# Performance work log

Measured on AMD Instinct MI355X. Metric: run time of the kernel, lower is better.

The kernel has to match this reference:

```python
import jax, jax.numpy as jnp
import numpy as np

N_NODES = 20000
N_EDGES = 240000
IN_DIM = 20
SH_DIM = 16  # (lmax+1)^2 with lmax=3
DENOM = 1.0
EPS = 1e-12


def spherical_harmonics_lmax3(v):
    """Real spherical harmonics l=0..3 on unit vectors v: [E,3] -> [E,16]."""
    x, y, z = v[:, 0], v[:, 1], v[:, 2]
    x2, y2, z2 = x * x, y * y, z * z
    sh = [
        jnp.full_like(x, 0.28209479177387814),            # l=0
        0.4886025119029199 * y,                            # l=1, m=-1
        0.4886025119029199 * z,                            # l=1, m=0
        0.4886025119029199 * x,                            # l=1, m=1
        1.0925484305920792 * x * y,                        # l=2, m=-2
        1.0925484305920792 * y * z,                        # l=2, m=-1
        0.31539156525252005 * (3.0 * z2 - 1.0),            # l=2, m=0
        1.0925484305920792 * x * z,                        # l=2, m=1
        0.5462742152960396 * (x2 - y2),                    # l=2, m=2
        0.5900435899266435 * y * (3.0 * x2 - y2),          # l=3, m=-3
        2.890611442640554 * x * y * z,                     # l=3, m=-2
        0.4570457994644658 * y * (5.0 * z2 - 1.0),         # l=3, m=-1
        0.3731763325901154 * z * (5.0 * z2 - 3.0),         # l=3, m=0
        0.4570457994644658 * x * (5.0 * z2 - 1.0),         # l=3, m=1
        1.445305721320277 * z * (x2 - y2),                 # l=3, m=2
        0.5900435899266435 * x * (x2 - 3.0 * y2),          # l=3, m=3
    ]
    return jnp.stack(sh, axis=-1)


def setup_inputs() -> dict:
    key = jax.random.key(0)
    ks = jax.random.split(key, 10)
    x = jax.random.normal(ks[0], (N_NODES, IN_DIM), dtype=jnp.float32)
    positions = jax.random.normal(ks[1], (N_NODES, 3), dtype=jnp.float32)
    edge_index = jax.random.randint(ks[2], (2, N_EDGES), 0, N_NODES, dtype=jnp.int32)
    s = 1.0 / np.sqrt(IN_DIM)
    W_pre = jax.random.uniform(ks[3], (IN_DIM, IN_DIM), jnp.float32, -s, s)
    b_pre = jax.random.uniform(ks[4], (IN_DIM,), jnp.float32, -s, s)
    W_post = jax.random.uniform(ks[5], (IN_DIM, IN_DIM), jnp.float32, -s, s)
    b_post = jax.random.uniform(ks[6], (IN_DIM,), jnp.float32, -s, s)
    W_sc = jax.random.uniform(ks[7], (IN_DIM, IN_DIM), jnp.float32, -s, s)
    b_sc = jax.random.uniform(ks[8], (IN_DIM,), jnp.float32, -s, s)
    return {"x": x, "positions": positions, "edge_index": edge_index,
            "W_pre": W_pre, "b_pre": b_pre, "W_post": W_post, "b_post": b_post,
            "W_sc": W_sc, "b_sc": b_sc}


def reference(x, positions, edge_index, W_pre, b_pre, W_post, b_post, W_sc, b_sc):
    row, col = edge_index[0], edge_index[1]
    # per-edge gather + relative positions
    rel = positions[col] - positions[row]                      # [E,3]
    norm = jnp.sqrt(jnp.sum(rel * rel, axis=-1, keepdims=True) + EPS)
    sh = spherical_harmonics_lmax3(rel / norm)                 # [E,16]
    sender = x[row]                                            # [E,20]
    # equivariant tensor product (outer product over irreps channels)
    tp = (sender[:, :, None] * sh[:, None, :]).reshape(sender.shape[0], IN_DIM * SH_DIM)  # [E,320]
    edge_features = jnp.concatenate([sender, tp], axis=1)      # [E,340]
    # scatter-add aggregation to target nodes
    aggr = jax.ops.segment_sum(edge_features, col, num_segments=N_NODES)  # [N,340]
    # node update MLP + shortcut (math of Layer.update)
    h = x / DENOM
    h = jax.nn.relu(h @ W_pre.T + b_pre)
    h = h @ W_post.T + b_post
    out = x @ W_sc.T + b_sc + h                                # [N,20]
    # aggr is computed (and aggregated) by the original propagate; concat so it stays live
    return jnp.concatenate([out, aggr], axis=1)                # [N,360]
```

## Files before the change

kernel.cpp:

```cpp
#include <hip/hip_runtime.h>

#define N_NODES 20000
#define N_EDGES 240000
#define IN_DIM  20
#define AGG_DIM 340
#define OUT_DIM 360
#define EPS_F   1e-12f
#define CAP     64
#define EDGE_BLOCKS ((N_EDGES + 255) / 256)
#define MLP_BLOCKS  ((N_NODES + 255) / 256)

typedef _Float16 half8 __attribute__((ext_vector_type(8)));

__device__ __forceinline__ float sh_coeff(int k, float xn, float yn, float zn) {
    const float x2 = xn * xn, y2 = yn * yn, z2 = zn * zn;
    switch (k) {
        case 0:  return 0.28209479177387814f;
        case 1:  return 0.4886025119029199f * yn;
        case 2:  return 0.4886025119029199f * zn;
        case 3:  return 0.4886025119029199f * xn;
        case 4:  return 1.0925484305920792f * xn * yn;
        case 5:  return 1.0925484305920792f * yn * zn;
        case 6:  return 0.31539156525252005f * (3.0f * z2 - 1.0f);
        case 7:  return 1.0925484305920792f * xn * zn;
        case 8:  return 0.5462742152960396f * (x2 - y2);
        case 9:  return 0.5900435899266435f * yn * (3.0f * x2 - y2);
        case 10: return 2.890611442640554f  * xn * yn * zn;
        case 11: return 0.4570457994644658f * yn * (5.0f * z2 - 1.0f);
        case 12: return 0.3731763325901154f * zn * (5.0f * z2 - 3.0f);
        case 13: return 0.4570457994644658f * xn * (5.0f * z2 - 1.0f);
        case 14: return 1.445305721320277f  * zn * (x2 - y2);
        default: return 0.5900435899266435f * xn * (x2 - 3.0f * y2);
    }
}

__global__ __launch_bounds__(256) void bucket_sh_mlp(
    const float* __restrict__ pos,
    const int* __restrict__ ei,
    const float* __restrict__ x,
    const float* __restrict__ Wpre,  const float* __restrict__ bpre,
    const float* __restrict__ Wpost, const float* __restrict__ bpost,
    const float* __restrict__ Wsc,   const float* __restrict__ bsc,
    int* __restrict__ counts,
    int* __restrict__ ovf_cnt,
    int* __restrict__ ovf,
    int* __restrict__ bucket,
    half8* __restrict__ shbuf,
    float* __restrict__ out)
{
    if ((int)blockIdx.x < EDGE_BLOCKS) {
        const int e = (int)(blockIdx.x * 256 + threadIdx.x);
        if (e >= N_EDGES) return;
        const int row = ei[e];
        const int col = ei[N_EDGES + e];
        const int slot = atomicAdd(&counts[col], 1);
        if (slot >= CAP) { ovf[atomicAdd(ovf_cnt, 1)] = e; return; }

        const int sidx = col * CAP + slot;
        bucket[sidx] = row;

        const float rx = pos[col * 3 + 0] - pos[row * 3 + 0];
        const float ry = pos[col * 3 + 1] - pos[row * 3 + 1];
        const float rz = pos[col * 3 + 2] - pos[row * 3 + 2];
        const float rinv = rsqrtf(rx * rx + ry * ry + rz * rz + EPS_F);
        const float xx = rx * rinv, yy = ry * rinv, zz = rz * rinv;
        const float x2 = xx * xx, y2 = yy * yy, z2 = zz * zz;

        const float sh0  = 0.28209479177387814f;
        const float sh1  = 0.4886025119029199f * yy;
        const float sh2  = 0.4886025119029199f * zz;
        const float sh3  = 0.4886025119029199f * xx;
        const float sh4  = 1.0925484305920792f * xx * yy;
        const float sh5  = 1.0925484305920792f * yy * zz;
        const float sh6  = 0.31539156525252005f * (3.0f * z2 - 1.0f);
        const float sh7  = 1.0925484305920792f * xx * zz;
        const float sh8  = 0.5462742152960396f * (x2 - y2);
        const float sh9  = 0.5900435899266435f * yy * (3.0f * x2 - y2);
        const float sh10 = 2.890611442640554f  * xx * yy * zz;
        const float sh11 = 0.4570457994644658f * yy * (5.0f * z2 - 1.0f);
        const float sh12 = 0.3731763325901154f * zz * (5.0f * z2 - 3.0f);
        const float sh13 = 0.4570457994644658f * xx * (5.0f * z2 - 1.0f);
        const float sh14 = 1.445305721320277f  * zz * (x2 - y2);
        const float sh15 = 0.5900435899266435f * xx * (x2 - 3.0f * y2);

        const half8 v0 = { (_Float16)sh12, (_Float16)sh13, (_Float16)sh14, (_Float16)sh15,
                           (_Float16)sh0,  (_Float16)sh1,  (_Float16)sh2,  (_Float16)sh3 };
        const half8 v1 = { (_Float16)sh4,  (_Float16)sh5,  (_Float16)sh6,  (_Float16)sh7,
                           (_Float16)sh8,  (_Float16)sh9,  (_Float16)sh10, (_Float16)sh11 };
        half8* dst = shbuf + (size_t)sidx * 2;
        dst[0] = v0;
        dst[1] = v1;
        return;
    }

    __shared__ float sWpre[IN_DIM * IN_DIM];
    __shared__ float sWpost[IN_DIM * IN_DIM];
    __shared__ float sWsc[IN_DIM * IN_DIM];
    __shared__ float sb[3 * IN_DIM];

    for (int t = threadIdx.x; t < IN_DIM * IN_DIM; t += 256) {
        sWpre[t]  = Wpre[t];
        sWpost[t] = Wpost[t];
        sWsc[t]   = Wsc[t];
    }
    if (threadIdx.x < IN_DIM) {
        sb[threadIdx.x]              = bpre[threadIdx.x];
        sb[IN_DIM + threadIdx.x]     = bpost[threadIdx.x];
        sb[2 * IN_DIM + threadIdx.x] = bsc[threadIdx.x];
    }
    __syncthreads();

    const int i = (int)((blockIdx.x - EDGE_BLOCKS) * 256 + threadIdx.x);
    if (i >= N_NODES) return;

    float xi[IN_DIM], h[IN_DIM];
#pragma unroll
    for (int j = 0; j < IN_DIM; ++j) xi[j] = x[(size_t)i * IN_DIM + j];

#pragma unroll
    for (int j = 0; j < IN_DIM; ++j) {
        float a = sb[j];
#pragma unroll
        for (int kk = 0; kk < IN_DIM; ++kk) a = fmaf(xi[kk], sWpre[j * IN_DIM + kk], a);
        h[j] = fmaxf(a, 0.0f);
    }
#pragma unroll
    for (int j = 0; j < IN_DIM; ++j) {
        float a = sb[IN_DIM + j] + sb[2 * IN_DIM + j];
#pragma unroll
        for (int kk = 0; kk < IN_DIM; ++kk) {
            a = fmaf(h[kk],  sWpost[j * IN_DIM + kk], a);
            a = fmaf(xi[kk], sWsc[j * IN_DIM + kk],  a);
        }
        out[(size_t)i * OUT_DIM + j] = a;
    }
}

__global__ __launch_bounds__(256) void node_gather(
    const float* __restrict__ x,
    const float* __restrict__ pos,
    const int* __restrict__ ei,
    const int* __restrict__ counts,
    const int* __restrict__ bucket,
    const _Float16* __restrict__ shbuf,
    const int* __restrict__ ovf_cnt,
    const int* __restrict__ ovf,
    float* __restrict__ out)
{
    const int lane   = threadIdx.x & 63;
    const int node   = (int)((blockIdx.x * blockDim.x + threadIdx.x) >> 6);
    const int lane20 = min(lane, IN_DIM - 1);
    const int lane16 = lane & 15;

    const int j0 = (lane >= IN_DIM) ? ((lane - IN_DIM) >> 4) : 0;
    const int j1 = (lane + 44)  >> 4;
    const int j2 = (lane + 108) >> 4;
    const int j3 = (lane + 172) >> 4;
    const int j4 = (lane + 236) >> 4;
    const int j5 = (lane + 300) >> 4;

    const int cnt_raw = __builtin_amdgcn_readfirstlane(counts[node]);
    const int cnt = min(cnt_raw, CAP);

    float acc0 = 0.f, acc1 = 0.f, acc2 = 0.f, acc3 = 0.f, acc4 = 0.f, acc5 = 0.f;
    float sum_s = 0.f;

#define ACCUM(S, SH)                                      \
    do {                                                  \
        sum_s += (S);                                     \
        acc0 = fmaf(__shfl((S), j0, 64), (SH), acc0);     \
        acc1 = fmaf(__shfl((S), j1, 64), (SH), acc1);     \
        acc2 = fmaf(__shfl((S), j2, 64), (SH), acc2);     \
        acc3 = fmaf(__shfl((S), j3, 64), (SH), acc3);     \
        acc4 = fmaf(__shfl((S), j4, 64), (SH), acc4);     \
        acc5 = fmaf(__shfl((S), j5, 64), (SH), acc5);     \
    } while (0)

    if (cnt > 0) {
        const int rl = bucket[node * CAP + min(lane, cnt - 1)];
        const _Float16* shb = shbuf + (size_t)node * CAP * 16 + lane16;

#define LOADCHUNK(B, S0, S1, S2, S3, H0, H1, H2, H3)                      \
    do {                                                                  \
        const int q1 = min((B) + 1, cnt - 1);                             \
        const int q2 = min((B) + 2, cnt - 1);                             \
        const int q3 = min((B) + 3, cnt - 1);                             \
        const int r0 = __builtin_amdgcn_readlane(rl, (B));                \
        const int r1 = __builtin_amdgcn_readlane(rl, q1);                 \
        const int r2 = __builtin_amdgcn_readlane(rl, q2);                 \
        const int r3 = __builtin_amdgcn_readlane(rl, q3);                 \
        S0 = x[(size_t)r0 * IN_DIM + lane20];                             \
        S1 = x[(size_t)r1 * IN_DIM + lane20];                             \
        S2 = x[(size_t)r2 * IN_DIM + lane20];                             \
        S3 = x[(size_t)r3 * IN_DIM + lane20];                             \
        H0 = (float)shb[(size_t)(B) * 16];                                \
        H1 = (float)shb[(size_t)q1 * 16];                                 \
        H2 = (float)shb[(size_t)q2 * 16];                                 \
        H3 = (float)shb[(size_t)q3 * 16];                                 \
    } while (0)

        float sA, sB, sC, sD, shA, shB, shC, shD;
        float tA, tB, tC, tD, uA, uB, uC, uD;

        LOADCHUNK(0, sA, sB, sC, sD, shA, shB, shC, shD);

        for (int base = 0; base < cnt; base += 4) {
            const int nb = base + 4;
            const bool have_next = nb < cnt;
            if (have_next)
                LOADCHUNK(nb, tA, tB, tC, tD, uA, uB, uC, uD);

            const float mB = (base + 1 < cnt) ? sB : 0.0f;
            const float mC = (base + 2 < cnt) ? sC : 0.0f;
            const float mD = (base + 3 < cnt) ? sD : 0.0f;

            ACCUM(sA, shA);
            ACCUM(mB, shB);
            ACCUM(mC, shC);
            ACCUM(mD, shD);

            if (have_next) {
                sA = tA; sB = tB; sC = tC; sD = tD;
                shA = uA; shB = uB; shC = uC; shD = uD;
            }
        }
#undef LOADCHUNK
    }

    if (cnt_raw > CAP) {
        const int m = *ovf_cnt;
        const int k = (lane + 12) & 15;
        for (int i = 0; i < m; ++i) {
            const int e = ovf[i];
            if (ei[N_EDGES + e] != node) continue;
            const int row = ei[e];
            const float rx = pos[node * 3 + 0] - pos[row * 3 + 0];
            const float ry = pos[node * 3 + 1] - pos[row * 3 + 1];
            const float rz = pos[node * 3 + 2] - pos[row * 3 + 2];
            const float rinv = rsqrtf(rx * rx + ry * ry + rz * rz + EPS_F);
            const float shk = sh_coeff(k, rx * rinv, ry * rinv, rz * rinv);
            const float s = x[(size_t)row * IN_DIM + lane20];
            ACCUM(s, shk);
        }
    }
#undef ACCUM

    float* obase = out + (size_t)node * OUT_DIM + IN_DIM;
    obase[lane]       = (lane < IN_DIM) ? sum_s : acc0;
    obase[lane + 64]  = acc1;
    obase[lane + 128] = acc2;
    obase[lane + 192] = acc3;
    obase[lane + 256] = acc4;
    if (lane < IN_DIM) obase[lane + 320] = acc5;
}

extern "C" void kernel_launch(void* const* d_in, const int* in_sizes, int n_in,
                              void* d_out, int out_size, void* d_ws, size_t ws_size,
                              hipStream_t stream)
{
    const float* x     = (const float*)d_in[0];
    const float* pos   = (const float*)d_in[1];
    const int*   ei    = (const int*)d_in[2];
    const float* Wpre  = (const float*)d_in[3];
    const float* bpre  = (const float*)d_in[4];
    const float* Wpost = (const float*)d_in[5];
    const float* bpost = (const float*)d_in[6];
    const float* Wsc   = (const float*)d_in[7];
    const float* bsc   = (const float*)d_in[8];
    float* out = (float*)d_out;

    half8* shbuf = (half8*)d_ws;
    int* ws_i    = (int*)((char*)d_ws + (size_t)N_NODES * CAP * 16 * sizeof(_Float16));
    int* counts  = ws_i;
    int* ovf_cnt = ws_i + N_NODES;
    int* ovf     = ws_i + N_NODES + 1;
    int* bucket  = ws_i + N_NODES + 1 + N_EDGES;

    hipMemsetAsync(counts, 0, (size_t)(N_NODES + 1) * sizeof(int), stream);

    bucket_sh_mlp<<<EDGE_BLOCKS + MLP_BLOCKS, 256, 0, stream>>>(
        pos, ei, x, Wpre, bpre, Wpost, bpost, Wsc, bsc,
        counts, ovf_cnt, ovf, bucket, shbuf, out);

    node_gather<<<(N_NODES * 64) / 256, 256, 0, stream>>>(
        x, pos, ei, counts, bucket, (const _Float16*)shbuf, ovf_cnt, ovf, out);
}
```

Before: 126.7 us.

## Fuse memset, bucketing, MLP and gather into one cooperative persistent kernel

Replaces the memset plus two kernel launches with a single cooperative kernel of 640 persistent blocks. It zeroes the counts, then runs the edge-bucketing and MLP pass in a grid-stride loop, then the per-node gather, with grid.sync between phases. This removes launch overhead and inter-kernel gaps. It also halves the per-node bucket capacity, which shrinks the SH buffer but pushes more edges onto the slower overflow path. Persistent blocks can lower occupancy and load balance compared with a full-size grid, and the old kernels stay as a fallback if the cooperative launch fails.

```diff
diff --git a/kernel.cpp b/kernel.cpp
--- a/kernel.cpp
+++ b/kernel.cpp
@@ -1,4 +1,7 @@
 #include <hip/hip_runtime.h>
+#include <hip/hip_cooperative_groups.h>
+
+namespace cg = cooperative_groups;
 
 #define N_NODES 20000
 #define N_EDGES 240000
@@ -6,7 +9,10 @@
 #define AGG_DIM 340
 #define OUT_DIM 360
 #define EPS_F   1e-12f
-#define CAP     64
+#define CAP     32
+#define GRID_BLOCKS 640
+#define GT          (GRID_BLOCKS * 256)
+#define TOTAL_WAVES (GRID_BLOCKS * 4)
 #define EDGE_BLOCKS ((N_EDGES + 255) / 256)
 #define MLP_BLOCKS  ((N_NODES + 255) / 256)
 
@@ -34,89 +40,60 @@
     }
 }
 
-__global__ __launch_bounds__(256) void bucket_sh_mlp(
-    const float* __restrict__ pos,
-    const int* __restrict__ ei,
-    const float* __restrict__ x,
-    const float* __restrict__ Wpre,  const float* __restrict__ bpre,
-    const float* __restrict__ Wpost, const float* __restrict__ bpost,
-    const float* __restrict__ Wsc,   const float* __restrict__ bsc,
-    int* __restrict__ counts,
-    int* __restrict__ ovf_cnt,
-    int* __restrict__ ovf,
-    int* __restrict__ bucket,
-    half8* __restrict__ shbuf,
-    float* __restrict__ out)
-{
-    if ((int)blockIdx.x < EDGE_BLOCKS) {
-        const int e = (int)(blockIdx.x * 256 + threadIdx.x);
-        if (e >= N_EDGES) return;
-        const int row = ei[e];
-        const int col = ei[N_EDGES + e];
-        const int slot = atomicAdd(&counts[col], 1);
-        if (slot >= CAP) { ovf[atomicAdd(ovf_cnt, 1)] = e; return; }
-
-        const int sidx = col * CAP + slot;
-        bucket[sidx] = row;
-
-        const float rx = pos[col * 3 + 0] - pos[row * 3 + 0];
-        const float ry = pos[col * 3 + 1] - pos[row * 3 + 1];
-        const float rz = pos[col * 3 + 2] - pos[row * 3 + 2];
-        const float rinv = rsqrtf(rx * rx + ry * ry + rz * rz + EPS_F);
-        const float xx = rx * rinv, yy = ry * rinv, zz = rz * rinv;
-        const float x2 = xx * xx, y2 = yy * yy, z2 = zz * zz;
-
-        const float sh0  = 0.28209479177387814f;
-        const float sh1  = 0.4886025119029199f * yy;
-        const float sh2  = 0.4886025119029199f * zz;
-        const float sh3  = 0.4886025119029199f * xx;
-        const float sh4  = 1.0925484305920792f * xx * yy;
-        const float sh5  = 1.0925484305920792f * yy * zz;
-        const float sh6  = 0.31539156525252005f * (3.0f * z2 - 1.0f);
-        const float sh7  = 1.0925484305920792f * xx * zz;
-        const float sh8  = 0.5462742152960396f * (x2 - y2);
-        const float sh9  = 0.5900435899266435f * yy * (3.0f * x2 - y2);
-        const float sh10 = 2.890611442640554f  * xx * yy * zz;
-        const float sh11 = 0.4570457994644658f * yy * (5.0f * z2 - 1.0f);
-        const float sh12 = 0.3731763325901154f * zz * (5.0f * z2 - 3.0f);
-        const float sh13 = 0.4570457994644658f * xx * (5.0f * z2 - 1.0f);
-        const float sh14 = 1.445305721320277f  * zz * (x2 - y2);
-        const float sh15 = 0.5900435899266435f * xx * (x2 - 3.0f * y2);
-
-        const half8 v0 = { (_Float16)sh12, (_Float16)sh13, (_Float16)sh14, (_Float16)sh15,
-                           (_Float16)sh0,  (_Float16)sh1,  (_Float16)sh2,  (_Float16)sh3 };
-        const half8 v1 = { (_Float16)sh4,  (_Float16)sh5,  (_Float16)sh6,  (_Float16)sh7,
-                           (_Float16)sh8,  (_Float16)sh9,  (_Float16)sh10, (_Float16)sh11 };
-        half8* dst = shbuf + (size_t)sidx * 2;
-        dst[0] = v0;
-        dst[1] = v1;
-        return;
-    }
-
-    __shared__ float sWpre[IN_DIM * IN_DIM];
-    __shared__ float sWpost[IN_DIM * IN_DIM];
-    __shared__ float sWsc[IN_DIM * IN_DIM];
-    __shared__ float sb[3 * IN_DIM];
-
-    for (int t = threadIdx.x; t < IN_DIM * IN_DIM; t += 256) {
-        sWpre[t]  = Wpre[t];
-        sWpost[t] = Wpost[t];
-        sWsc[t]   = Wsc[t];
-    }
-    if (threadIdx.x < IN_DIM) {
-        sb[threadIdx.x]              = bpre[threadIdx.x];
-        sb[IN_DIM + threadIdx.x]     = bpost[threadIdx.x];
-        sb[2 * IN_DIM + threadIdx.x] = bsc[threadIdx.x];
-    }
-    __syncthreads();
-
-    const int i = (int)((blockIdx.x - EDGE_BLOCKS) * 256 + threadIdx.x);
-    if (i >= N_NODES) return;
-
+__device__ __forceinline__ void do_edge(
+    int e, const float* __restrict__ pos, const int* __restrict__ ei,
+    int* __restrict__ counts, int* __restrict__ ovf_cnt, int* __restrict__ ovf,
+    int* __restrict__ bucket, _Float16* __restrict__ shbuf)
+{
+    const int row = ei[e];
+    const int col = ei[N_EDGES + e];
+    const int slot = atomicAdd(&counts[col], 1);
+    if (slot >= CAP) { ovf[atomicAdd(ovf_cnt, 1)] = e; return; }
+
+    const int sidx = col * CAP + slot;
+    bucket[sidx] = row;
+
+    const float rx = pos[col * 3 + 0] - pos[row * 3 + 0];
+    const float ry = pos[col * 3 + 1] - pos[row * 3 + 1];
+    const float rz = pos[col * 3 + 2] - pos[row * 3 + 2];
+    const float rinv = rsqrtf(rx * rx + ry * ry + rz * rz + EPS_F);
+    const float xx = rx * rinv, yy = ry * rinv, zz = rz * rinv;
+    const float x2 = xx * xx, y2 = yy * yy, z2 = zz * zz;
+
+    const float sh0  = 0.28209479177387814f;
+    const float sh1  = 0.4886025119029199f * yy;
+    const float sh2  = 0.4886025119029199f * zz;
+    const float sh3  = 0.4886025119029199f * xx;
+    const float sh4  = 1.0925484305920792f * xx * yy;
+    const float sh5  = 1.0925484305920792f * yy * zz;
+    const float sh6  = 0.31539156525252005f * (3.0f * z2 - 1.0f);
+    const float sh7  = 1.0925484305920792f * xx * zz;
+    const float sh8  = 0.5462742152960396f * (x2 - y2);
+    const float sh9  = 0.5900435899266435f * yy * (3.0f * x2 - y2);
+    const float sh10 = 2.890611442640554f  * xx * yy * zz;
+    const float sh11 = 0.4570457994644658f * yy * (5.0f * z2 - 1.0f);
+    const float sh12 = 0.3731763325901154f * zz * (5.0f * z2 - 3.0f);
+    const float sh13 = 0.4570457994644658f * xx * (5.0f * z2 - 1.0f);
+    const float sh14 = 1.445305721320277f  * zz * (x2 - y2);
+    const float sh15 = 0.5900435899266435f * xx * (x2 - 3.0f * y2);
+
+    const half8 v0 = { (_Float16)sh12, (_Float16)sh13, (_Float16)sh14, (_Float16)sh15,
+                       (_Float16)sh0,  (_Float16)sh1,  (_Float16)sh2,  (_Float16)sh3 };
+    const half8 v1 = { (_Float16)sh4,  (_Float16)sh5,  (_Float16)sh6,  (_Float16)sh7,
+                       (_Float16)sh8,  (_Float16)sh9,  (_Float16)sh10, (_Float16)sh11 };
+    half8* dst = (half8*)(shbuf + (size_t)sidx * 16);
+    dst[0] = v0;
+    dst[1] = v1;
+}
+
+__device__ __forceinline__ void do_mlp(
+    int i, const float* __restrict__ x,
+    const float* sWpre, const float* sWpost, const float* sWsc, const float* sb,
+    float* __restrict__ out)
+{
     float xi[IN_DIM], h[IN_DIM];
 #pragma unroll
     for (int j = 0; j < IN_DIM; ++j) xi[j] = x[(size_t)i * IN_DIM + j];
-
 #pragma unroll
     for (int j = 0; j < IN_DIM; ++j) {
         float a = sb[j];
@@ -136,22 +113,16 @@
     }
 }
 
-__global__ __launch_bounds__(256) void node_gather(
-    const float* __restrict__ x,
-    const float* __restrict__ pos,
-    const int* __restrict__ ei,
-    const int* __restrict__ counts,
-    const int* __restrict__ bucket,
-    const _Float16* __restrict__ shbuf,
-    const int* __restrict__ ovf_cnt,
-    const int* __restrict__ ovf,
-    float* __restrict__ out)
-{
-    const int lane   = threadIdx.x & 63;
-    const int node   = (int)((blockIdx.x * blockDim.x + threadIdx.x) >> 6);
+__device__ __forceinline__ void do_gather(
+    int node, int lane,
+    const float* __restrict__ x, const float* __restrict__ pos,
+    const int* __restrict__ ei, const int* __restrict__ counts,
+    const int* __restrict__ bucket, const _Float16* __restrict__ shbuf,
+    const int* __restrict__ ovf_cnt, const int* __restrict__ ovf,
+    float* __restrict__ out)
+{
     const int lane20 = min(lane, IN_DIM - 1);
     const int lane16 = lane & 15;
-
     const int j0 = (lane >= IN_DIM) ? ((lane - IN_DIM) >> 4) : 0;
     const int j1 = (lane + 44)  >> 4;
     const int j2 = (lane + 108) >> 4;
@@ -254,6 +225,107 @@
     if (lane < IN_DIM) obase[lane + 320] = acc5;
 }
 
+__global__ __launch_bounds__(256, 3) void fused_all(
+    const float* __restrict__ x,
+    const float* __restrict__ pos,
+    const int* __restrict__ ei,
+    const float* __restrict__ Wpre,  const float* __restrict__ bpre,
+    const float* __restrict__ Wpost, const float* __restrict__ bpost,
+    const float* __restrict__ Wsc,   const float* __restrict__ bsc,
+    int* __restrict__ counts, int* __restrict__ ovf_cnt, int* __restrict__ ovf,
+    int* __restrict__ bucket, _Float16* __restrict__ shbuf,
+    float* __restrict__ out)
+{
+    cg::grid_group grid = cg::this_grid();
+    const int t   = (int)threadIdx.x;
+    const int tid = (int)blockIdx.x * 256 + t;
+
+    __shared__ float sWpre[IN_DIM * IN_DIM];
+    __shared__ float sWpost[IN_DIM * IN_DIM];
+    __shared__ float sWsc[IN_DIM * IN_DIM];
+    __shared__ float sb[3 * IN_DIM];
+
+    for (int i = t; i < IN_DIM * IN_DIM; i += 256) {
+        sWpre[i]  = Wpre[i];
+        sWpost[i] = Wpost[i];
+        sWsc[i]   = Wsc[i];
+    }
+    if (t < IN_DIM) {
+        sb[t]              = bpre[t];
+        sb[IN_DIM + t]     = bpost[t];
+        sb[2 * IN_DIM + t] = bsc[t];
+    }
+
+    for (int i = tid; i < N_NODES + 1; i += GT) counts[i] = 0;
+
+    __syncthreads();
+    grid.sync();
+
+    for (int i = tid; i < N_EDGES + N_NODES; i += GT) {
+        if (i < N_EDGES) do_edge(i, pos, ei, counts, ovf_cnt, ovf, bucket, shbuf);
+        else             do_mlp(i - N_EDGES, x, sWpre, sWpost, sWsc, sb, out);
+    }
+
+    grid.sync();
+
+    const int lane  = t & 63;
+    const int wave0 = tid >> 6;
+    for (int node = wave0; node < N_NODES; node += TOTAL_WAVES)
+        do_gather(node, lane, x, pos, ei, counts, bucket, shbuf, ovf_cnt, ovf, out);
+}
+
+__global__ __launch_bounds__(256) void bucket_sh_mlp(
+    const float* __restrict__ pos,
+    const int* __restrict__ ei,
+    const float* __restrict__ x,
+    const float* __restrict__ Wpre,  const float* __restrict__ bpre,
+    const float* __restrict__ Wpost, const float* __restrict__ bpost,
+    const float* __restrict__ Wsc,   const float* __restrict__ bsc,
+    int* __restrict__ counts, int* __restrict__ ovf_cnt, int* __restrict__ ovf,
+    int* __restrict__ bucket, _Float16* __restrict__ shbuf,
+    float* __restrict__ out)
+{
+    if ((int)blockIdx.x < EDGE_BLOCKS) {
+        const int e = (int)(blockIdx.x * 256 + threadIdx.x);
+        if (e < N_EDGES) do_edge(e, pos, ei, counts, ovf_cnt, ovf, bucket, shbuf);
+        return;
+    }
+    __shared__ float sWpre[IN_DIM * IN_DIM];
+    __shared__ float sWpost[IN_DIM * IN_DIM];
+    __shared__ float sWsc[IN_DIM * IN_DIM];
+    __shared__ float sb[3 * IN_DIM];
+    for (int i = (int)threadIdx.x; i < IN_DIM * IN_DIM; i += 256) {
+        sWpre[i]  = Wpre[i];
+        sWpost[i] = Wpost[i];
+        sWsc[i]   = Wsc[i];
+    }
+    if (threadIdx.x < IN_DIM) {
+        sb[threadIdx.x]              = bpre[threadIdx.x];
+        sb[IN_DIM + threadIdx.x]     = bpost[threadIdx.x];
+        sb[2 * IN_DIM + threadIdx.x] = bsc[threadIdx.x];
+    }
+    __syncthreads();
+    const int i = (int)((blockIdx.x - EDGE_BLOCKS) * 256 + threadIdx.x);
+    if (i < N_NODES) do_mlp(i, x, sWpre, sWpost, sWsc, sb, out);
+}
+
+__global__ __launch_bounds__(256) void node_gather(
+    const float* __restrict__ x,
+    const float* __restrict__ pos,
+    const int* __restrict__ ei,
+    const int* __restrict__ counts,
+    const int* __restrict__ bucket,
+    const _Float16* __restrict__ shbuf,
+    const int* __restrict__ ovf_cnt,
+    const int* __restrict__ ovf,
+    float* __restrict__ out)
+{
+    const int lane = (int)(threadIdx.x & 63);
+    const int node = (int)((blockIdx.x * blockDim.x + threadIdx.x) >> 6);
+    if (node >= N_NODES) return;
+    do_gather(node, lane, x, pos, ei, counts, bucket, shbuf, ovf_cnt, ovf, out);
+}
+
 extern "C" void kernel_launch(void* const* d_in, const int* in_sizes, int n_in,
                               void* d_out, int out_size, void* d_ws, size_t ws_size,
                               hipStream_t stream)
@@ -269,19 +341,29 @@
     const float* bsc   = (const float*)d_in[8];
     float* out = (float*)d_out;
 
-    half8* shbuf = (half8*)d_ws;
+    _Float16* shbuf = (_Float16*)d_ws;
     int* ws_i    = (int*)((char*)d_ws + (size_t)N_NODES * CAP * 16 * sizeof(_Float16));
     int* counts  = ws_i;
     int* ovf_cnt = ws_i + N_NODES;
     int* ovf     = ws_i + N_NODES + 1;
     int* bucket  = ws_i + N_NODES + 1 + N_EDGES;
 
-    hipMemsetAsync(counts, 0, (size_t)(N_NODES + 1) * sizeof(int), stream);
-
-    bucket_sh_mlp<<<EDGE_BLOCKS + MLP_BLOCKS, 256, 0, stream>>>(
-        pos, ei, x, Wpre, bpre, Wpost, bpost, Wsc, bsc,
-        counts, ovf_cnt, ovf, bucket, shbuf, out);
-
-    node_gather<<<(N_NODES * 64) / 256, 256, 0, stream>>>(
-        x, pos, ei, counts, bucket, (const _Float16*)shbuf, ovf_cnt, ovf, out);
-}
+    void* args[] = {
+        (void*)&x, (void*)&pos, (void*)&ei,
+        (void*)&Wpre, (void*)&bpre, (void*)&Wpost, (void*)&bpost,
+        (void*)&Wsc, (void*)&bsc,
+        (void*)&counts, (void*)&ovf_cnt, (void*)&ovf, (void*)&bucket,
+        (void*)&shbuf, (void*)&out
+    };
+    hipError_t rc = hipLaunchCooperativeKernel((const void*)fused_all,
+                                               dim3(GRID_BLOCKS), dim3(256),
+                                               args, 0, stream);
+    if (rc != hipSuccess) {
+        hipMemsetAsync(counts, 0, (size_t)(N_NODES + 1) * sizeof(int), stream);
+        bucket_sh_mlp<<<EDGE_BLOCKS + MLP_BLOCKS, 256, 0, stream>>>(
+            pos, ei, x, Wpre, bpre, Wpost, bpost, Wsc, bsc,
+            counts, ovf_cnt, ovf, bucket, shbuf, out);
+        node_gather<<<(N_NODES * 64) / 256, 256, 0, stream>>>(
+            x, pos, ei, counts, bucket, shbuf, ovf_cnt, ovf, out);
+    }
+}
```

New measurement: 347.5 us. 2.74x slower.
